# Optimization experiments

Hardware: AMD Instinct MI355X
Metric: run time of the kernel (lower is better)

## Reference

```python
import jax, jax.numpy as jnp
import numpy as np


def setup_inputs() -> dict:
    key = jax.random.key(0)
    kx, kw = jax.random.split(key)
    A_MAX = 16  # activations in [0, 2**A_bits - 1] = [0, 15]
    W_MAX = 15  # torch.randint(0, 2**W_bits - 1) -> [0, 14]
    x = jax.random.randint(kx, (32, 256, 56, 56), 0, A_MAX, dtype=jnp.int32)
    weight = jax.random.randint(kw, (256, 256, 3, 3), 0, W_MAX, dtype=jnp.int32)
    return {"x": x, "weight": weight}


def reference(x, weight):
    # Low-bit quantized conv2d: direct_conv2d(x.int(), w.int(), stride=1) with the
    # module's crop for (k=3, padding=1) is equivalent to a conv with padding=1.
    # Max accumulator value = 15*14*9*256 < 2**24, so fp32 accumulation is exact.
    xf = x.astype(jnp.float32)
    wf = weight.astype(jnp.float32)
    y = jax.lax.conv_general_dilated(
        xf, wf,
        window_strides=(1, 1),
        padding=((1, 1), (1, 1)),
        dimension_numbers=("NCHW", "OIHW", "NCHW"),
    )
    return y.astype(jnp.int32)  # [32, 256, 56, 56]
```

## Files before the change

### kernel.cpp

```cpp
#include <hip/hip_runtime.h>

typedef int v4i  __attribute__((ext_vector_type(4)));
typedef int v16i __attribute__((ext_vector_type(16)));

#define N_IMG   32
#define C_IN    256
#define HWDIM   56
#define HW2     3136
#define OUT_TOT 25690112
#define OUT_NSTR 802816

#define PXB     272
#define PPI     3364
#define XP_IMG  915008
#define XP_SLACK 4096
#define WP_CB2STR 73728
#define WP_BYTES  589824ull

#define S_TILE  64
#define TILES_PER_IMG 49
#define WIN_B   50048

__global__ void dc_x_to_nhwc(const int* __restrict__ x, unsigned int* __restrict__ x8,
                             int n0) {
    __shared__ unsigned int lds[64 * 65];
    const int t = threadIdx.x;
    const int w = t & 63, q = t >> 6;
    const int nl = blockIdx.x / HWDIM, h = blockIdx.x % HWDIM;

    if (w < HWDIM) {
        const int* xb = x + (size_t)(n0 + nl) * OUT_NSTR + h * HWDIM + w;
        #pragma unroll
        for (int it = 0; it < 16; ++it) {
            const int cg4 = q * 16 + it;
            const int ci0 = cg4 * 4;
            unsigned v  =  ((unsigned)xb[(ci0 + 0) * HW2] & 0xff);
            v |= ((unsigned)xb[(ci0 + 1) * HW2] & 0xff) << 8;
            v |= ((unsigned)xb[(ci0 + 2) * HW2] & 0xff) << 16;
            v |= ((unsigned)xb[(ci0 + 3) * HW2] & 0xff) << 24;
            lds[w * 65 + cg4] = v;
        }
    }
    __syncthreads();
    unsigned int* ob = x8 + (size_t)nl * (PPI * (PXB / 4)) + ((h + 1) * 58 + 1) * (PXB / 4);
    #pragma unroll
    for (int it = 0; it < 14; ++it) {
        const int f = it * 256 + t;
        const int w2 = f >> 6, cg = f & 63;
        if (w2 < HWDIM) ob[w2 * (PXB / 4) + cg] = lds[w2 * 65 + cg];
    }
}

__global__ void dc_halo(unsigned int* __restrict__ x8) {
    const int nl = blockIdx.x;
    const int t = threadIdx.x;
    if (t < 228) {
        int h, w;
        if (t < 58)       { h = 0;        w = t; }
        else if (t < 116) { h = 57;       w = t - 58; }
        else if (t < 172) { h = t - 115;  w = 0; }
        else              { h = t - 171;  w = 57; }
        unsigned int* p = x8 + ((size_t)nl * PPI + h * 58 + w) * (PXB / 4);
        #pragma unroll
        for (int i = 0; i < PXB / 4; ++i) p[i] = 0;
    }
}

__global__ void dc_pack_w(const int* __restrict__ wt, unsigned int* __restrict__ wp) {
    const int tid = blockIdx.x * 256 + threadIdx.x;
    const int jq = tid & 3;
    const int l  = (tid >> 2) & 63;
    const int kb = (tid >> 8) & 7;
    const int r  = tid >> 11;
    const int t  = r % 9;
    const int cb2 = r / 9;
    const int co  = cb2 * 32 + (l & 31);
    const int ci0 = kb * 32 + (l >> 5) * 16 + jq * 4;
    const int kh = t / 3, kw = t - kh * 3;
    unsigned v = 0;
    #pragma unroll
    for (int k = 0; k < 4; ++k) {
        unsigned b = (unsigned)wt[((co * C_IN + ci0 + k) * 3 + kh) * 3 + kw];
        v |= (b & 0xff) << (8 * k);
    }
    wp[tid] = v;
}

__device__ __forceinline__ void gll16(const char* g, char* l) {
    __builtin_amdgcn_global_load_lds(
        (const __attribute__((address_space(1))) unsigned int*)g,
        (__attribute__((address_space(3))) unsigned int*)l, 16, 0, 0);
}

__global__ __launch_bounds__(512, 6) void dc_mfma(const char* __restrict__ x8,
                                                  const char* __restrict__ wp,
                                                  int* __restrict__ out, int nwg) {
    extern __shared__ __align__(16) char xs[];

    const int bid = blockIdx.x;
    const int q = nwg >> 3, r = nwg & 7;
    const int xcd = bid & 7, bidx = bid >> 3;
    const int wgid = (xcd < r ? xcd * (q + 1) : r * (q + 1) + (xcd - r) * q) + bidx;

    const int nl = wgid / TILES_PER_IMG, st = wgid - nl * TILES_PER_IMG;

    const int tid = threadIdx.x;
    const int l = tid & 63, wid = tid >> 6;
    const int lane31 = l & 31, hi = l >> 5;

    const int hw0 = st * S_TILE;
    const int h0 = hw0 / HWDIM, w0 = hw0 - h0 * HWDIM;
    const int p0 = h0 * 58 + w0;
    const char* gsrc = x8 + (size_t)nl * XP_IMG + (size_t)p0 * PXB;

    #pragma unroll
    for (int c = 0; c < 7; ++c) {
        const int off = (c * 512 + tid) * 16;
        if (off < WIN_B) gll16(gsrc + off, xs + off);
    }

    int breg[2], outb[2];
    #pragma unroll
    for (int ni = 0; ni < 2; ++ni) {
        const int hw = hw0 + ni * 32 + lane31;
        const int h = hw / HWDIM, w = hw - h * HWDIM;
        const int p = (h + 1) * 58 + (w + 1);
        breg[ni] = (p - p0) * PXB + hi * 16 - 16048;
        outb[ni] = nl * OUT_NSTR + hw;
    }

    const char* wb = wp + wid * WP_CB2STR + l * 16;

    const int xoffp[9] = {
        16048 - 59 * PXB, 16048 - 58 * PXB, 16048 - 57 * PXB,
        16048 - 1 * PXB,  16048,            16048 + 1 * PXB,
        16048 + 57 * PXB, 16048 + 58 * PXB, 16048 + 59 * PXB
    };

    __syncthreads();

    v16i acc[2] = {};
    v4i wa[3];

    wa[0] = *(const v4i*)(wb);
    wa[1] = *(const v4i*)(wb + 1024);

    #pragma unroll
    for (int j = 0; j < 72; ++j) {
        const int jc = j % 3;
        if (j + 2 < 72)
            wa[(j + 2) % 3] = *(const v4i*)(wb + (j + 2) * 1024);

        const int t = j >> 3, kb = j & 7;
        const int xo = xoffp[t] + kb * 32;
        const v4i xf0 = *(const v4i*)(xs + breg[0] + xo);
        const v4i xf1 = *(const v4i*)(xs + breg[1] + xo);

        __builtin_amdgcn_s_setprio(1);
        acc[0] = __builtin_amdgcn_mfma_i32_32x32x32_i8(wa[jc], xf0, acc[0], 0, 0, 0);
        acc[1] = __builtin_amdgcn_mfma_i32_32x32x32_i8(wa[jc], xf1, acc[1], 0, 0, 0);
        __builtin_amdgcn_s_setprio(0);
    }

    #pragma unroll
    for (int ni = 0; ni < 2; ++ni) {
        const v16i c = acc[ni];
        int* ob = out + outb[ni] + (wid * 32 + 4 * hi) * HW2;
        #pragma unroll
        for (int rr = 0; rr < 16; ++rr) {
            __builtin_nontemporal_store(c[rr], ob + ((rr & 3) + 8 * (rr >> 2)) * HW2);
        }
    }
}

__global__ void dc_naive(const int* __restrict__ x, const int* __restrict__ wt,
                         int* __restrict__ out) {
    const int idx = blockIdx.x * 256 + threadIdx.x;
    if (idx >= OUT_TOT) return;
    const int w = idx % HWDIM;
    const int h = (idx / HWDIM) % HWDIM;
    const int co = (idx / HW2) & 255;
    const int n = idx / OUT_NSTR;
    const int* xn = x + n * OUT_NSTR;
    const int* wo = wt + co * (C_IN * 9);
    int acc = 0;
    for (int ci = 0; ci < C_IN; ++ci) {
        const int* xc = xn + ci * HW2;
        const int* wc = wo + ci * 9;
        #pragma unroll
        for (int kh = 0; kh < 3; ++kh) {
            const int hh = h + kh - 1;
            if ((unsigned)hh >= HWDIM) continue;
            #pragma unroll
            for (int kw = 0; kw < 3; ++kw) {
                const int ww = w + kw - 1;
                if ((unsigned)ww >= HWDIM) continue;
                acc += xc[hh * HWDIM + ww] * wc[kh * 3 + kw];
            }
        }
    }
    out[idx] = acc;
}

extern "C" void kernel_launch(void* const* d_in, const int* in_sizes, int n_in,
                              void* d_out, int out_size, void* d_ws, size_t ws_size,
                              hipStream_t stream) {
    const int* x  = (const int*)d_in[0];
    const int* wt = (const int*)d_in[1];
    int* out = (int*)d_out;

    int chunk = 0;
    const int cand[4] = {32, 16, 8, 4};
    for (int i = 0; i < 4; ++i) {
        if ((size_t)cand[i] * XP_IMG + XP_SLACK + WP_BYTES <= ws_size) { chunk = cand[i]; break; }
    }

    if (chunk > 0) {
        char* x8 = (char*)d_ws;
        const size_t x8_bytes = (size_t)chunk * XP_IMG + XP_SLACK;
        unsigned int* wp = (unsigned int*)(x8 + x8_bytes);
        hipLaunchKernelGGL(dc_halo, dim3(chunk), dim3(256), 0, stream, (unsigned int*)x8);
        hipLaunchKernelGGL(dc_pack_w, dim3(576), dim3(256), 0, stream, wt, wp);
        for (int n0 = 0; n0 < N_IMG; n0 += chunk) {
            hipLaunchKernelGGL(dc_x_to_nhwc, dim3(chunk * HWDIM), dim3(256), 0, stream,
                               x, (unsigned int*)x8, n0);
            const int nwg = chunk * TILES_PER_IMG;
            hipLaunchKernelGGL(dc_mfma, dim3(nwg), dim3(512), WIN_B, stream,
                               (const char*)x8, (const char*)wp,
                               out + (size_t)n0 * OUT_NSTR, nwg);
        }
        return;
    }

    hipLaunchKernelGGL(dc_naive, dim3((OUT_TOT + 255) / 256), dim3(256), 0, stream,
                       x, wt, out);
}
```

Baseline: 99.14 us.

## Enlarge conv tile to 128 pixels and 64 output channels per wave

After: 116.8 us. 17.8% more time.

```diff
diff --git a/kernel.cpp b/kernel.cpp
--- a/kernel.cpp
+++ b/kernel.cpp
@@ -13,13 +13,13 @@
 #define PXB     272
 #define PPI     3364
 #define XP_IMG  915008
-#define XP_SLACK 4096
+#define XP_SLACK 69632
 #define WP_CB2STR 73728
 #define WP_BYTES  589824ull
 
-#define S_TILE  64
-#define TILES_PER_IMG 49
-#define WIN_B   50048
+#define S_TILE  128
+#define TILES_PER_IMG 25
+#define WIN_B   68544
 
 __global__ void dc_x_to_nhwc(const int* __restrict__ x, unsigned int* __restrict__ x8,
                              int n0) {
@@ -92,7 +92,7 @@
         (__attribute__((address_space(3))) unsigned int*)l, 16, 0, 0);
 }
 
-__global__ __launch_bounds__(512, 6) void dc_mfma(const char* __restrict__ x8,
+__global__ __launch_bounds__(256, 2) void dc_mfma(const char* __restrict__ x8,
                                                   const char* __restrict__ wp,
                                                   int* __restrict__ out, int nwg) {
     extern __shared__ __align__(16) char xs[];
@@ -114,22 +114,26 @@
     const char* gsrc = x8 + (size_t)nl * XP_IMG + (size_t)p0 * PXB;
 
     #pragma unroll
-    for (int c = 0; c < 7; ++c) {
-        const int off = (c * 512 + tid) * 16;
+    for (int c = 0; c < 17; ++c) {
+        const int off = (c * 256 + tid) * 16;
         if (off < WIN_B) gll16(gsrc + off, xs + off);
     }
 
-    int breg[2], outb[2];
-    #pragma unroll
-    for (int ni = 0; ni < 2; ++ni) {
-        const int hw = hw0 + ni * 32 + lane31;
+    int breg[4], outb[4];
+    bool val[4];
+    #pragma unroll
+    for (int ni = 0; ni < 4; ++ni) {
+        int hw = hw0 + ni * 32 + lane31;
+        val[ni] = (hw < HW2);
+        if (!val[ni]) hw = HW2 - 1;
         const int h = hw / HWDIM, w = hw - h * HWDIM;
         const int p = (h + 1) * 58 + (w + 1);
         breg[ni] = (p - p0) * PXB + hi * 16 - 16048;
         outb[ni] = nl * OUT_NSTR + hw;
     }
 
-    const char* wb = wp + wid * WP_CB2STR + l * 16;
+    const char* wb0 = wp + (wid * 2) * WP_CB2STR + l * 16;
+    const char* wb1 = wb0 + WP_CB2STR;
 
     const int xoffp[9] = {
         16048 - 59 * PXB, 16048 - 58 * PXB, 16048 - 57 * PXB,
@@ -139,36 +143,40 @@
 
     __syncthreads();
 
-    v16i acc[2] = {};
-    v4i wa[3];
-
-    wa[0] = *(const v4i*)(wb);
-    wa[1] = *(const v4i*)(wb + 1024);
+    v16i acc[2][4] = {};
 
     #pragma unroll
     for (int j = 0; j < 72; ++j) {
-        const int jc = j % 3;
-        if (j + 2 < 72)
-            wa[(j + 2) % 3] = *(const v4i*)(wb + (j + 2) * 1024);
-
         const int t = j >> 3, kb = j & 7;
         const int xo = xoffp[t] + kb * 32;
-        const v4i xf0 = *(const v4i*)(xs + breg[0] + xo);
-        const v4i xf1 = *(const v4i*)(xs + breg[1] + xo);
+
+        const v4i wf0 = *(const v4i*)(wb0 + j * 1024);
+        const v4i wf1 = *(const v4i*)(wb1 + j * 1024);
+        v4i xf[4];
+        #pragma unroll
+        for (int ni = 0; ni < 4; ++ni)
+            xf[ni] = *(const v4i*)(xs + breg[ni] + xo);
 
         __builtin_amdgcn_s_setprio(1);
-        acc[0] = __builtin_amdgcn_mfma_i32_32x32x32_i8(wa[jc], xf0, acc[0], 0, 0, 0);
-        acc[1] = __builtin_amdgcn_mfma_i32_32x32x32_i8(wa[jc], xf1, acc[1], 0, 0, 0);
+        #pragma unroll
+        for (int ni = 0; ni < 4; ++ni) {
+            acc[0][ni] = __builtin_amdgcn_mfma_i32_32x32x32_i8(wf0, xf[ni], acc[0][ni], 0, 0, 0);
+            acc[1][ni] = __builtin_amdgcn_mfma_i32_32x32x32_i8(wf1, xf[ni], acc[1][ni], 0, 0, 0);
+        }
         __builtin_amdgcn_s_setprio(0);
     }
 
     #pragma unroll
-    for (int ni = 0; ni < 2; ++ni) {
-        const v16i c = acc[ni];
-        int* ob = out + outb[ni] + (wid * 32 + 4 * hi) * HW2;
-        #pragma unroll
-        for (int rr = 0; rr < 16; ++rr) {
-            __builtin_nontemporal_store(c[rr], ob + ((rr & 3) + 8 * (rr >> 2)) * HW2);
+    for (int mi = 0; mi < 2; ++mi) {
+        #pragma unroll
+        for (int ni = 0; ni < 4; ++ni) {
+            if (!val[ni]) continue;
+            const v16i c = acc[mi][ni];
+            int* ob = out + outb[ni] + (wid * 64 + mi * 32 + 4 * hi) * HW2;
+            #pragma unroll
+            for (int rr = 0; rr < 16; ++rr) {
+                __builtin_nontemporal_store(c[rr], ob + ((rr & 3) + 8 * (rr >> 2)) * HW2);
+            }
         }
     }
 }
@@ -225,7 +233,7 @@
             hipLaunchKernelGGL(dc_x_to_nhwc, dim3(chunk * HWDIM), dim3(256), 0, stream,
                                x, (unsigned int*)x8, n0);
             const int nwg = chunk * TILES_PER_IMG;
-            hipLaunchKernelGGL(dc_mfma, dim3(nwg), dim3(512), WIN_B, stream,
+            hipLaunchKernelGGL(dc_mfma, dim3(nwg), dim3(256), WIN_B, stream,
                                (const char*)x8, (const char*)wp,
                                out + (size_t)n0 * OUT_NSTR, nwg);
         }
```
